# Kernel tuning notes

Measured on AMD Instinct MI355X. Metric: run time of the kernel, lower is better.

Reference implementation:

```python
import jax, jax.numpy as jnp
import numpy as np

NUM_CHIPS = 4
EXPERTS_PER_CHIP = 8
N_EXPERTS = 32            # NUM_CHIPS * EXPERTS_PER_CHIP
TOP_K = 4
SEQ = 1024
HIDDEN = 2048
MAX_TOK = 1024            # max_dispatched_tokens_per_expert
META_LEN = 8


def setup_inputs() -> dict:
    key = jax.random.key(0)
    k1, k2, k3 = jax.random.split(key, 3)
    x = jax.random.normal(k1, (NUM_CHIPS, SEQ, HIDDEN), jnp.float32)
    weights = jax.random.uniform(k2, (NUM_CHIPS, SEQ, TOP_K), jnp.float32)
    indices = jax.random.randint(k3, (NUM_CHIPS, SEQ, TOP_K), 0, N_EXPERTS, jnp.int32)
    return {"x": x, "weights": weights, "indices": indices}


def _dispatch_plan(indices):
    """Compute, for every (chip, token, topk) assignment, its destination slot in the
    global per-expert buffers, replicating the serialized offset-counter loop:
    chips write in order chip0..chipC, and within a chip in (token, topk) order."""
    C, S, K = indices.shape
    N = S * K
    e = indices.reshape(C, N)                                     # expert per assignment
    # per-chip per-expert counts
    counts = jax.vmap(lambda ec: jnp.zeros(N_EXPERTS, jnp.int32).at[ec].add(1))(e)  # [C,E]
    # exclusive prefix sum over chips -> starting offset of each chip within each expert buffer
    chip_off = jnp.cumsum(counts, axis=0) - counts                # [C,E]

    def rank_within_chip(ec, cnt):
        # stable sort groups assignments by expert while preserving (token, topk) order
        order = jnp.argsort(ec, stable=True)
        group_start = (jnp.cumsum(cnt) - cnt)[ec[order]]
        rk_sorted = jnp.arange(N, dtype=jnp.int32) - group_start
        return jnp.zeros(N, jnp.int32).at[order].set(rk_sorted)

    rank = jax.vmap(rank_within_chip)(e, counts)                  # [C,N]
    dst = jnp.take_along_axis(chip_off, e, axis=1) + rank         # slot within expert buffer
    flat = (e * MAX_TOK + dst).reshape(-1)                        # index into (E*MAX_TOK)
    return e, flat, counts


def reference(x, weights, indices):
    C, S, H = x.shape
    K = indices.shape[-1]
    N = S * K
    e, flat, counts = _dispatch_plan(indices)

    # scatter token vectors: each assignment gets a unique slot -> plain set
    x_rep = jnp.repeat(x, K, axis=1).reshape(C * N, H)
    buf = jnp.zeros((N_EXPERTS * MAX_TOK, H), x.dtype).at[flat].set(x_rep)
    buf = buf.reshape(NUM_CHIPS, EXPERTS_PER_CHIP, MAX_TOK, H)

    # metadata: [chip, token, topk, routed_expert, bf16-bits(weight), 0...]
    chip_id = jnp.broadcast_to(jnp.arange(C, dtype=jnp.int32)[:, None], (C, N))
    tok = jnp.broadcast_to(jnp.repeat(jnp.arange(S, dtype=jnp.int32), K)[None, :], (C, N))
    topk = jnp.broadcast_to(jnp.tile(jnp.arange(K, dtype=jnp.int32), S)[None, :], (C, N))
    wbits = jax.lax.bitcast_convert_type(weights.astype(jnp.bfloat16), jnp.int16)
    wbits = wbits.astype(jnp.int32).reshape(C, N)
    md = jnp.stack([chip_id, tok, topk, e, wbits], axis=-1)       # [C,N,5]
    md = jnp.concatenate([md, jnp.zeros((C, N, META_LEN - 5), jnp.int32)], axis=-1)
    meta = jnp.full((N_EXPERTS * MAX_TOK, META_LEN), -1, jnp.int32).at[flat].set(md.reshape(-1, META_LEN))
    meta = meta.reshape(NUM_CHIPS, EXPERTS_PER_CHIP, MAX_TOK, META_LEN)

    experts_counter = counts.sum(axis=0).reshape(NUM_CHIPS, EXPERTS_PER_CHIP)
    return buf, meta, experts_counter
```

## Files before the change

kernel.cpp:

```cpp
#include <hip/hip_runtime.h>
#include <hip/hip_bf16.h>
#include <stdint.h>
#include <string.h>

#define NUM_CHIPS 4
#define N_EXPERTS 32
#define TOP_K 4
#define SEQ 1024
#define HIDDEN 2048
#define MAX_TOK 1024
#define META_LEN 8
#define NPC (SEQ * TOP_K)
#define NTOT (NUM_CHIPS * NPC)
#define ROWS (N_EXPERTS * MAX_TOK)
#define BUF_ELEMS ((size_t)ROWS * HIDDEN)
#define META_OFF BUF_ELEMS
#define CNT_OFF (BUF_ELEMS + (size_t)ROWS * META_LEN)

#define WS_RANK 0
#define WS_CNT  (NTOT)
#define WS_TOT  (NTOT + 128)
#define WS_INV  (NTOT + 128 + 32)

typedef float vfloat4 __attribute__((ext_vector_type(4)));

__global__ __launch_bounds__(1024) void rank_kernel(const int* __restrict__ idx,
                                                    int* __restrict__ ws) {
    __shared__ int run_base[N_EXPERTS];
    __shared__ int wave_cnt[16][N_EXPERTS];
    __shared__ int wave_base[16][N_EXPERTS];

    const int c = blockIdx.x;
    const int t = threadIdx.x;
    const int lane = t & 63;
    const int w = t >> 6;

    int e[4];
#pragma unroll
    for (int q = 0; q < 4; ++q) e[q] = idx[c * NPC + q * 1024 + t];

    if (t < N_EXPERTS) run_base[t] = 0;
    __syncthreads();

#pragma unroll
    for (int q = 0; q < 4; ++q) {
        if (t < 16 * N_EXPERTS) ((int*)wave_cnt)[t] = 0;
        __syncthreads();

        uint64_t m = ~0ull;
#pragma unroll
        for (int b = 0; b < 5; ++b) {
            uint64_t bb = __ballot((e[q] >> b) & 1);
            m &= ((e[q] >> b) & 1) ? bb : ~bb;
        }
        const int rk = __popcll(m & ((1ull << lane) - 1ull));
        if (rk == 0) wave_cnt[w][e[q]] = __popcll(m);
        __syncthreads();

        if (t < N_EXPERTS) {
            int s = run_base[t];
#pragma unroll
            for (int ww = 0; ww < 16; ++ww) {
                wave_base[ww][t] = s;
                s += wave_cnt[ww][t];
            }
            run_base[t] = s;
        }
        __syncthreads();

        ws[WS_RANK + c * NPC + q * 1024 + t] = wave_base[w][e[q]] + rk;
    }
    __syncthreads();
    if (t < N_EXPERTS) ws[WS_CNT + c * N_EXPERTS + t] = run_base[t];
}

__global__ __launch_bounds__(256) void emit_kernel(const int* __restrict__ idx,
                                                   int* __restrict__ ws,
                                                   float* __restrict__ out) {
    __shared__ int cnt_s[NUM_CHIPS * N_EXPERTS];
    const int t = threadIdx.x;
    if (t < NUM_CHIPS * N_EXPERTS) cnt_s[t] = ws[WS_CNT + t];
    __syncthreads();

    const int a = blockIdx.x * 256 + t;
    const int c = a >> 12;
    const int n = a & (NPC - 1);
    const int e = idx[a];

    int off = 0;
    for (int cc = 0; cc < c; ++cc) off += cnt_s[cc * N_EXPERTS + e];
    const int dst = off + ws[WS_RANK + a];
    ws[WS_INV + e * MAX_TOK + dst] = (c << 12) | n;

    if (blockIdx.x == 0 && t < N_EXPERTS) {
        int s = cnt_s[t] + cnt_s[N_EXPERTS + t] + cnt_s[2 * N_EXPERTS + t] +
                cnt_s[3 * N_EXPERTS + t];
        ws[WS_TOT + t] = s;
        out[CNT_OFF + t] = (float)s;
    }
}

__global__ __launch_bounds__(256) void scatter_kernel(const float* __restrict__ x,
                                                      const float* __restrict__ wts,
                                                      const int* __restrict__ ws,
                                                      float* __restrict__ out) {
    const int t = threadIdx.x;
    const int row0 = blockIdx.x * 4;
    const int e = row0 >> 10;
    const int slot0 = row0 & (MAX_TOK - 1);

    const int tot = ws[WS_TOT + e];

    int iv[4];
    bool occ[4];
#pragma unroll
    for (int r = 0; r < 4; ++r) {
        occ[r] = (slot0 + r) < tot;
        iv[r] = occ[r] ? ws[WS_INV + row0 + r] : 0;
    }

    vfloat4 v[4][2];
#pragma unroll
    for (int r = 0; r < 4; ++r) {
        if (occ[r]) {
            const int c = iv[r] >> 12;
            const int n = iv[r] & (NPC - 1);
            const vfloat4* src =
                (const vfloat4*)(x + ((size_t)c * SEQ + (n >> 2)) * HIDDEN);
            v[r][0] = src[t];
            v[r][1] = src[t + 256];
        } else {
            v[r][0] = (vfloat4)(0.f);
            v[r][1] = (vfloat4)(0.f);
        }
    }

#pragma unroll
    for (int r = 0; r < 4; ++r) {
        vfloat4* dst = (vfloat4*)(out + (size_t)(row0 + r) * HIDDEN);
        __builtin_nontemporal_store(v[r][0], dst + t);
        __builtin_nontemporal_store(v[r][1], dst + t + 256);

        if (t < META_LEN) {
            float mv = -1.0f;
            if (occ[r]) {
                const int c = iv[r] >> 12;
                const int n = iv[r] & (NPC - 1);
                mv = 0.0f;
                if (t == 0) mv = (float)c;
                else if (t == 1) mv = (float)(n >> 2);
                else if (t == 2) mv = (float)(n & 3);
                else if (t == 3) mv = (float)e;
                else if (t == 4) {
                    float wv = wts[c * NPC + n];
                    uint32_t ub;
                    memcpy(&ub, &wv, 4);
                    uint32_t lsb = (ub >> 16) & 1u;
                    uint32_t bits = (ub + 0x7FFFu + lsb) >> 16;
                    mv = (float)(int)(short)(uint16_t)bits;
                }
            }
            __builtin_nontemporal_store(
                mv, out + META_OFF + (size_t)(row0 + r) * META_LEN + t);
        }
    }
}

extern "C" void kernel_launch(void* const* d_in, const int* in_sizes, int n_in,
                              void* d_out, int out_size, void* d_ws, size_t ws_size,
                              hipStream_t stream) {
    const float* x   = (const float*)d_in[0];
    const float* wts = (const float*)d_in[1];
    const int*   idx = (const int*)d_in[2];
    float* out = (float*)d_out;
    int* ws = (int*)d_ws;

    rank_kernel<<<NUM_CHIPS, 1024, 0, stream>>>(idx, ws);
    emit_kernel<<<NTOT / 256, 256, 0, stream>>>(idx, ws, out);
    scatter_kernel<<<ROWS / 4, 256, 0, stream>>>(x, wts, ws, out);
}
```

Before: 303.4 us.

## Scatter per source token instead of gathering per destination row

Replaces the inverse-map emit kernel and the per-row gather with a forward scatter. Each block reads one token row once and writes it to its TOP_K destination slots. A separate kernel zero-fills and writes -1 metadata only for the unoccupied slots. This drops the inverse-index pass and reads each source row once instead of once per assignment, but the writes now land in scattered rows and the two output kernels must cover disjoint regions exactly.

```diff
diff --git a/kernel.cpp b/kernel.cpp
--- a/kernel.cpp
+++ b/kernel.cpp
@@ -19,8 +19,6 @@
 
 #define WS_RANK 0
 #define WS_CNT  (NTOT)
-#define WS_TOT  (NTOT + 128)
-#define WS_INV  (NTOT + 128 + 32)
 
 typedef float vfloat4 __attribute__((ext_vector_type(4)));
 
@@ -74,95 +72,89 @@
     if (t < N_EXPERTS) ws[WS_CNT + c * N_EXPERTS + t] = run_base[t];
 }
 
-__global__ __launch_bounds__(256) void emit_kernel(const int* __restrict__ idx,
-                                                   int* __restrict__ ws,
+__global__ __launch_bounds__(256) void scatter_occ(const float* __restrict__ x,
+                                                   const float* __restrict__ wts,
+                                                   const int* __restrict__ idx,
+                                                   const int* __restrict__ ws,
                                                    float* __restrict__ out) {
     __shared__ int cnt_s[NUM_CHIPS * N_EXPERTS];
     const int t = threadIdx.x;
+    const int b = blockIdx.x;
+    const int c = b >> 10;
+    const int tk = b & (SEQ - 1);
+
     if (t < NUM_CHIPS * N_EXPERTS) cnt_s[t] = ws[WS_CNT + t];
+
+    const vfloat4* src = (const vfloat4*)(x + ((size_t)c * SEQ + tk) * HIDDEN);
+    vfloat4 v0 = src[t];
+    vfloat4 v1 = src[t + 256];
+
+    int e[TOP_K], rk[TOP_K];
+#pragma unroll
+    for (int k = 0; k < TOP_K; ++k) {
+        e[k] = idx[c * NPC + tk * TOP_K + k];
+        rk[k] = ws[WS_RANK + c * NPC + tk * TOP_K + k];
+    }
     __syncthreads();
 
-    const int a = blockIdx.x * 256 + t;
-    const int c = a >> 12;
-    const int n = a & (NPC - 1);
-    const int e = idx[a];
+#pragma unroll
+    for (int k = 0; k < TOP_K; ++k) {
+        int off = 0;
+        for (int cc = 0; cc < c; ++cc) off += cnt_s[cc * N_EXPERTS + e[k]];
+        const int row = e[k] * MAX_TOK + off + rk[k];
 
-    int off = 0;
-    for (int cc = 0; cc < c; ++cc) off += cnt_s[cc * N_EXPERTS + e];
-    const int dst = off + ws[WS_RANK + a];
-    ws[WS_INV + e * MAX_TOK + dst] = (c << 12) | n;
+        vfloat4* dst = (vfloat4*)(out + (size_t)row * HIDDEN);
+        __builtin_nontemporal_store(v0, dst + t);
+        __builtin_nontemporal_store(v1, dst + t + 256);
 
-    if (blockIdx.x == 0 && t < N_EXPERTS) {
-        int s = cnt_s[t] + cnt_s[N_EXPERTS + t] + cnt_s[2 * N_EXPERTS + t] +
-                cnt_s[3 * N_EXPERTS + t];
-        ws[WS_TOT + t] = s;
-        out[CNT_OFF + t] = (float)s;
+        if (t < META_LEN) {
+            float mv = 0.0f;
+            if (t == 0) mv = (float)c;
+            else if (t == 1) mv = (float)tk;
+            else if (t == 2) mv = (float)k;
+            else if (t == 3) mv = (float)e[k];
+            else if (t == 4) {
+                float wv = wts[c * NPC + tk * TOP_K + k];
+                uint32_t ub;
+                memcpy(&ub, &wv, 4);
+                uint32_t lsb = (ub >> 16) & 1u;
+                uint32_t bits = (ub + 0x7FFFu + lsb) >> 16;
+                mv = (float)(int)(short)(uint16_t)bits;
+            }
+            __builtin_nontemporal_store(
+                mv, out + META_OFF + (size_t)row * META_LEN + t);
+        }
     }
 }
 
-__global__ __launch_bounds__(256) void scatter_kernel(const float* __restrict__ x,
-                                                      const float* __restrict__ wts,
-                                                      const int* __restrict__ ws,
-                                                      float* __restrict__ out) {
+__global__ __launch_bounds__(256) void scatter_empty(const int* __restrict__ ws,
+                                                     float* __restrict__ out) {
     const int t = threadIdx.x;
     const int row0 = blockIdx.x * 4;
     const int e = row0 >> 10;
     const int slot0 = row0 & (MAX_TOK - 1);
 
-    const int tot = ws[WS_TOT + e];
+    const int tot = ws[WS_CNT + e] + ws[WS_CNT + N_EXPERTS + e] +
+                    ws[WS_CNT + 2 * N_EXPERTS + e] + ws[WS_CNT + 3 * N_EXPERTS + e];
 
-    int iv[4];
-    bool occ[4];
+    if (blockIdx.x == 0 && t < N_EXPERTS) {
+        int s = ws[WS_CNT + t] + ws[WS_CNT + N_EXPERTS + t] +
+                ws[WS_CNT + 2 * N_EXPERTS + t] + ws[WS_CNT + 3 * N_EXPERTS + t];
+        out[CNT_OFF + t] = (float)s;
+    }
+
+    if (slot0 + 3 < tot) return;
+
+    const vfloat4 z = (vfloat4)(0.f);
 #pragma unroll
     for (int r = 0; r < 4; ++r) {
-        occ[r] = (slot0 + r) < tot;
-        iv[r] = occ[r] ? ws[WS_INV + row0 + r] : 0;
-    }
-
-    vfloat4 v[4][2];
-#pragma unroll
-    for (int r = 0; r < 4; ++r) {
-        if (occ[r]) {
-            const int c = iv[r] >> 12;
-            const int n = iv[r] & (NPC - 1);
-            const vfloat4* src =
-                (const vfloat4*)(x + ((size_t)c * SEQ + (n >> 2)) * HIDDEN);
-            v[r][0] = src[t];
-            v[r][1] = src[t + 256];
-        } else {
-            v[r][0] = (vfloat4)(0.f);
-            v[r][1] = (vfloat4)(0.f);
-        }
-    }
-
-#pragma unroll
-    for (int r = 0; r < 4; ++r) {
+        if (slot0 + r < tot) continue;
         vfloat4* dst = (vfloat4*)(out + (size_t)(row0 + r) * HIDDEN);
-        __builtin_nontemporal_store(v[r][0], dst + t);
-        __builtin_nontemporal_store(v[r][1], dst + t + 256);
-
-        if (t < META_LEN) {
-            float mv = -1.0f;
-            if (occ[r]) {
-                const int c = iv[r] >> 12;
-                const int n = iv[r] & (NPC - 1);
-                mv = 0.0f;
-                if (t == 0) mv = (float)c;
-                else if (t == 1) mv = (float)(n >> 2);
-                else if (t == 2) mv = (float)(n & 3);
-                else if (t == 3) mv = (float)e;
-                else if (t == 4) {
-                    float wv = wts[c * NPC + n];
-                    uint32_t ub;
-                    memcpy(&ub, &wv, 4);
-                    uint32_t lsb = (ub >> 16) & 1u;
-                    uint32_t bits = (ub + 0x7FFFu + lsb) >> 16;
-                    mv = (float)(int)(short)(uint16_t)bits;
-                }
-            }
+        __builtin_nontemporal_store(z, dst + t);
+        __builtin_nontemporal_store(z, dst + t + 256);
+        if (t < META_LEN)
             __builtin_nontemporal_store(
-                mv, out + META_OFF + (size_t)(row0 + r) * META_LEN + t);
-        }
+                -1.0f, out + META_OFF + (size_t)(row0 + r) * META_LEN + t);
     }
 }
 
@@ -176,6 +168,6 @@
     int* ws = (int*)d_ws;
 
     rank_kernel<<<NUM_CHIPS, 1024, 0, stream>>>(idx, ws);
-    emit_kernel<<<NTOT / 256, 256, 0, stream>>>(idx, ws, out);
-    scatter_kernel<<<ROWS / 4, 256, 0, stream>>>(x, wts, ws, out);
+    scatter_empty<<<ROWS / 4, 256, 0, stream>>>(ws, out);
+    scatter_occ<<<NUM_CHIPS * SEQ, 256, 0, stream>>>(x, wts, idx, ws, out);
 }
```

Result: no change. 300.3 us (-1.0%).
